# Optimization experiments

Measured on AMD Instinct MI355X. Metric: run time of the kernel, lower is better.

## Reference

```python
import jax, jax.numpy as jnp
import numpy as np

D = 32  # latent_dim
# relation order for stacked params: 0=ss, 1=tt, 2=st, 3=ts

def setup_inputs() -> dict:
    key = jax.random.key(0)
    ks = jax.random.split(key, 6)
    B, N, T = 32, 1024, 256
    spatial_nodes = jax.random.normal(ks[0], (B, N, D), dtype=jnp.float32)
    temporal_nodes = jax.random.normal(ks[1], (B, T, D), dtype=jnp.float32)
    # Linear(2D, 1) weights for the 4 relation MLPs and 4 mask MLPs, stacked.
    scale = 1.0 / np.sqrt(2 * D)
    W_rel = jax.random.uniform(ks[2], (4, 2 * D), jnp.float32, -scale, scale)
    b_rel = jax.random.uniform(ks[3], (4,), jnp.float32, -scale, scale)
    W_mask = jax.random.uniform(ks[4], (4, 2 * D), jnp.float32, -scale, scale)
    b_mask = jax.random.uniform(ks[5], (4,), jnp.float32, -scale, scale)
    return {"spatial_nodes": spatial_nodes, "temporal_nodes": temporal_nodes,
            "W_rel": W_rel, "b_rel": b_rel, "W_mask": W_mask, "b_mask": b_mask}


def _sub_graph(x1, x2, w_rel, brel, w_mask, bmask):
    # Linear applied to concat(x1_i, x2_j) decomposes as x1_i@w[:D] + x2_j@w[D:] + b,
    # avoiding the O(B*N1*N2*2D) concat intermediate of the original code.
    a1 = x1 @ w_rel[:D]          # [B, N1]
    a2 = x2 @ w_rel[D:]          # [B, N2]
    adj = a1[:, :, None] + a2[:, None, :] + brel   # [B, N1, N2]
    m1 = x1 @ w_mask[:D]
    m2 = x2 @ w_mask[D:]
    mask = jax.nn.relu(m1[:, :, None] + m2[:, None, :] + bmask)
    return adj, mask


def reference(spatial_nodes, temporal_nodes, W_rel, b_rel, W_mask, b_mask):
    s, t = spatial_nodes, temporal_nodes
    ss_a, ss_m = _sub_graph(s, s, W_rel[0], b_rel[0], W_mask[0], b_mask[0])
    tt_a, tt_m = _sub_graph(t, t, W_rel[1], b_rel[1], W_mask[1], b_mask[1])
    st_a, st_m = _sub_graph(s, t, W_rel[2], b_rel[2], W_mask[2], b_mask[2])
    ts_a, ts_m = _sub_graph(t, s, W_rel[3], b_rel[3], W_mask[3], b_mask[3])
    adj = jnp.concatenate([
        jnp.concatenate([ss_a, st_a], axis=-1),
        jnp.concatenate([ts_a, tt_a], axis=-1)], axis=-2)   # [B, N+T, N+T]
    mask = jnp.concatenate([
        jnp.concatenate([ss_m, st_m], axis=-1),
        jnp.concatenate([ts_m, tt_m], axis=-1)], axis=-2)
    adj = jnp.tanh(adj * mask)
    # Per-batch sparse edge extraction (nonzero/gather) in the original has
    # data-dependent shapes; it is a pure re-indexing of adj's nonzeros and is
    # omitted from the jit-compatible dense reference output.
    return adj
```

## Files before the change

### kernel.cpp

```cpp
#include <hip/hip_runtime.h>
#include <hip/hip_bf16.h>
#include <cstddef>

#define D_  32
#define N_  1024
#define T_  256
#define NT_ 1280
#define B_  32
#define TI  128
#define TJ  256

__device__ __forceinline__ float fast_tanh(float x) {
    float e = __expf(2.0f * x);
    return 1.0f - 2.0f * __builtin_amdgcn_rcpf(e + 1.0f);
}

__global__ __launch_bounds__(256) void mlp_adj_kernel(
    const float* __restrict__ S,  const float* __restrict__ Tn,
    const float* __restrict__ Wr, const float* __restrict__ br,
    const float* __restrict__ Wm, const float* __restrict__ bm,
    float* __restrict__ out)
{
    __shared__ float rowA[TI], rowM[TI], colA[TJ], colM[TJ];

    const int jt = blockIdx.x % (NT_ / TJ);
    const int it = (blockIdx.x / (NT_ / TJ)) % (NT_ / TI);
    const int b  = blockIdx.x / ((NT_ / TJ) * (NT_ / TI));
    const int i0 = it * TI, j0 = jt * TJ;
    const int rr = (i0 >= N_);
    const int cc = (j0 >= N_);
    const int r  = rr ? (cc ? 1 : 3) : (cc ? 2 : 0);

    const float* wrR = Wr + r * 2 * D_;
    const float* wrC = wrR + D_;
    const float* wmR = Wm + r * 2 * D_;
    const float* wmC = wmR + D_;
    const float  brel  = br[r];
    const float  bmask = bm[r];
    const int    tid   = threadIdx.x;

    const float* Xrow = rr ? (Tn + ((size_t)b * T_ + (i0 - N_)) * D_)
                           : (S  + ((size_t)b * N_ +  i0       ) * D_);
    const float* Xcol = cc ? (Tn + ((size_t)b * T_ + (j0 - N_)) * D_)
                           : (S  + ((size_t)b * N_ +  j0       ) * D_);

    if (tid < TI) {
        const float4* x  = (const float4*)(Xrow + (size_t)tid * D_);
        const float4* wa = (const float4*)wrR;
        const float4* wq = (const float4*)wmR;
        float aA = brel, aM = bmask;
        #pragma unroll
        for (int k = 0; k < D_ / 4; ++k) {
            float4 xv = x[k], av = wa[k], mv = wq[k];
            aA = fmaf(xv.x, av.x, aA); aM = fmaf(xv.x, mv.x, aM);
            aA = fmaf(xv.y, av.y, aA); aM = fmaf(xv.y, mv.y, aM);
            aA = fmaf(xv.z, av.z, aA); aM = fmaf(xv.z, mv.z, aM);
            aA = fmaf(xv.w, av.w, aA); aM = fmaf(xv.w, mv.w, aM);
        }
        rowA[tid] = aA; rowM[tid] = aM;
    }
    {
        const float4* x  = (const float4*)(Xcol + (size_t)tid * D_);
        const float4* wa = (const float4*)wrC;
        const float4* wq = (const float4*)wmC;
        float aA = 0.f, aM = 0.f;
        #pragma unroll
        for (int k = 0; k < D_ / 4; ++k) {
            float4 xv = x[k], av = wa[k], mv = wq[k];
            aA = fmaf(xv.x, av.x, aA); aM = fmaf(xv.x, mv.x, aM);
            aA = fmaf(xv.y, av.y, aA); aM = fmaf(xv.y, mv.y, aM);
            aA = fmaf(xv.z, av.z, aA); aM = fmaf(xv.z, mv.z, aM);
            aA = fmaf(xv.w, av.w, aA); aM = fmaf(xv.w, mv.w, aM);
        }
        colA[tid] = aA; colM[tid] = aM;
    }
    __syncthreads();

    const int jq = (tid & 63) * 4;
    const int rb = tid >> 6;
    const float4 cA = *(const float4*)&colA[jq];
    const float4 cM = *(const float4*)&colM[jq];
    float* outp = out + ((size_t)b * NT_ + i0) * NT_ + j0 + jq;

    for (int i = rb; i < TI; i += 4) {
        const float ra = rowA[i], rm = rowM[i];
        float4 o;
        o.x = fast_tanh((ra + cA.x) * fmaxf(rm + cM.x, 0.f));
        o.y = fast_tanh((ra + cA.y) * fmaxf(rm + cM.y, 0.f));
        o.z = fast_tanh((ra + cA.z) * fmaxf(rm + cM.z, 0.f));
        o.w = fast_tanh((ra + cA.w) * fmaxf(rm + cM.w, 0.f));
        *(float4*)(outp + (size_t)i * NT_) = o;
    }
}

extern "C" void kernel_launch(void* const* d_in, const int* in_sizes, int n_in,
                              void* d_out, int out_size, void* d_ws, size_t ws_size,
                              hipStream_t stream) {
    const float* S  = (const float*)d_in[0];
    const float* Tn = (const float*)d_in[1];
    const float* Wr = (const float*)d_in[2];
    const float* br = (const float*)d_in[3];
    const float* Wm = (const float*)d_in[4];
    const float* bm = (const float*)d_in[5];
    float* out = (float*)d_out;

    const int grid = B_ * (NT_ / TI) * (NT_ / TJ);
    mlp_adj_kernel<<<grid, 256, 0, stream>>>(S, Tn, Wr, br, Wm, bm, out);
}
```

Before: 218.2 us.

## Retile into full-width row bands with per-band column projections and nontemporal stores

```diff
diff --git a/kernel.cpp b/kernel.cpp
--- a/kernel.cpp
+++ b/kernel.cpp
@@ -1,5 +1,4 @@
 #include <hip/hip_runtime.h>
-#include <hip/hip_bf16.h>
 #include <cstddef>
 
 #define D_  32
@@ -7,12 +6,30 @@
 #define T_  256
 #define NT_ 1280
 #define B_  32
-#define TI  128
-#define TJ  256
+#define RB  32
+#define NBANDS (NT_/RB)
+
+typedef float vf4 __attribute__((ext_vector_type(4)));
 
 __device__ __forceinline__ float fast_tanh(float x) {
     float e = __expf(2.0f * x);
     return 1.0f - 2.0f * __builtin_amdgcn_rcpf(e + 1.0f);
+}
+
+__device__ __forceinline__ float dot32(const float* __restrict__ x,
+                                       const float* __restrict__ w) {
+    const float4* xv = (const float4*)x;
+    const float4* wv = (const float4*)w;
+    float a = 0.f;
+    #pragma unroll
+    for (int k = 0; k < D_ / 4; ++k) {
+        float4 xx = xv[k], ww = wv[k];
+        a = fmaf(xx.x, ww.x, a);
+        a = fmaf(xx.y, ww.y, a);
+        a = fmaf(xx.z, ww.z, a);
+        a = fmaf(xx.w, ww.w, a);
+    }
+    return a;
 }
 
 __global__ __launch_bounds__(256) void mlp_adj_kernel(
@@ -21,75 +38,82 @@
     const float* __restrict__ Wm, const float* __restrict__ bm,
     float* __restrict__ out)
 {
-    __shared__ float rowA[TI], rowM[TI], colA[TJ], colM[TJ];
+    __shared__ float colA[NT_], colM[NT_];
+    __shared__ float rowP[4][RB];
 
-    const int jt = blockIdx.x % (NT_ / TJ);
-    const int it = (blockIdx.x / (NT_ / TJ)) % (NT_ / TI);
-    const int b  = blockIdx.x / ((NT_ / TJ) * (NT_ / TI));
-    const int i0 = it * TI, j0 = jt * TJ;
-    const int rr = (i0 >= N_);
-    const int cc = (j0 >= N_);
-    const int r  = rr ? (cc ? 1 : 3) : (cc ? 2 : 0);
-
-    const float* wrR = Wr + r * 2 * D_;
-    const float* wrC = wrR + D_;
-    const float* wmR = Wm + r * 2 * D_;
-    const float* wmC = wmR + D_;
-    const float  brel  = br[r];
-    const float  bmask = bm[r];
-    const int    tid   = threadIdx.x;
+    const int band = blockIdx.x % NBANDS;
+    const int b    = blockIdx.x / NBANDS;
+    const int i0   = band * RB;
+    const int rr   = (i0 >= N_);
+    const int r1   = rr ? 3 : 0;
+    const int r2   = rr ? 1 : 2;
+    const int tid  = threadIdx.x;
 
     const float* Xrow = rr ? (Tn + ((size_t)b * T_ + (i0 - N_)) * D_)
-                           : (S  + ((size_t)b * N_ +  i0       ) * D_);
-    const float* Xcol = cc ? (Tn + ((size_t)b * T_ + (j0 - N_)) * D_)
-                           : (S  + ((size_t)b * N_ +  j0       ) * D_);
+                           : (S  + ((size_t)b * N_ +  i0      ) * D_);
 
-    if (tid < TI) {
-        const float4* x  = (const float4*)(Xrow + (size_t)tid * D_);
-        const float4* wa = (const float4*)wrR;
-        const float4* wq = (const float4*)wmR;
-        float aA = brel, aM = bmask;
+    if (tid < 4 * RB) {
+        const int i     = tid & (RB - 1);
+        const int which = tid >> 5;
+        const int rsel  = (which & 2) ? r2 : r1;
+        const float* w  = ((which & 1) ? Wm : Wr) + rsel * 2 * D_;
+        rowP[which][i] = dot32(Xrow + (size_t)i * D_, w);
+    }
+
+    {
+        const float* wrC1 = Wr + r1 * 2 * D_ + D_;
+        const float* wmC1 = Wm + r1 * 2 * D_ + D_;
+        const float* wrC2 = Wr + r2 * 2 * D_ + D_;
+        const float* wmC2 = Wm + r2 * 2 * D_ + D_;
+        const float  bA1 = br[r1], bM1 = bm[r1], bA2 = br[r2], bM2 = bm[r2];
         #pragma unroll
-        for (int k = 0; k < D_ / 4; ++k) {
-            float4 xv = x[k], av = wa[k], mv = wq[k];
-            aA = fmaf(xv.x, av.x, aA); aM = fmaf(xv.x, mv.x, aM);
-            aA = fmaf(xv.y, av.y, aA); aM = fmaf(xv.y, mv.y, aM);
-            aA = fmaf(xv.z, av.z, aA); aM = fmaf(xv.z, mv.z, aM);
-            aA = fmaf(xv.w, av.w, aA); aM = fmaf(xv.w, mv.w, aM);
+        for (int c = 0; c < 4; ++c) {
+            const int j = c * 256 + tid;
+            const float* xj = S + ((size_t)b * N_ + j) * D_;
+            colA[j] = dot32(xj, wrC1) + bA1;
+            colM[j] = dot32(xj, wmC1) + bM1;
         }
-        rowA[tid] = aA; rowM[tid] = aM;
-    }
-    {
-        const float4* x  = (const float4*)(Xcol + (size_t)tid * D_);
-        const float4* wa = (const float4*)wrC;
-        const float4* wq = (const float4*)wmC;
-        float aA = 0.f, aM = 0.f;
-        #pragma unroll
-        for (int k = 0; k < D_ / 4; ++k) {
-            float4 xv = x[k], av = wa[k], mv = wq[k];
-            aA = fmaf(xv.x, av.x, aA); aM = fmaf(xv.x, mv.x, aM);
-            aA = fmaf(xv.y, av.y, aA); aM = fmaf(xv.y, mv.y, aM);
-            aA = fmaf(xv.z, av.z, aA); aM = fmaf(xv.z, mv.z, aM);
-            aA = fmaf(xv.w, av.w, aA); aM = fmaf(xv.w, mv.w, aM);
+        {
+            const float* xj = Tn + ((size_t)b * T_ + tid) * D_;
+            colA[1024 + tid] = dot32(xj, wrC2) + bA2;
+            colM[1024 + tid] = dot32(xj, wmC2) + bM2;
         }
-        colA[tid] = aA; colM[tid] = aM;
     }
     __syncthreads();
 
-    const int jq = (tid & 63) * 4;
-    const int rb = tid >> 6;
-    const float4 cA = *(const float4*)&colA[jq];
-    const float4 cM = *(const float4*)&colM[jq];
-    float* outp = out + ((size_t)b * NT_ + i0) * NT_ + j0 + jq;
+    const int l = tid & 63;
+    const int w = tid >> 6;
+    float4 cAv[5], cMv[5];
+    #pragma unroll
+    for (int c = 0; c < 5; ++c) {
+        cAv[c] = *(const float4*)&colA[c * 256 + l * 4];
+        cMv[c] = *(const float4*)&colM[c * 256 + l * 4];
+    }
+    const int rbase = w * 8;
+    float rA1[8], rM1[8], rA2[8], rM2[8];
+    #pragma unroll
+    for (int k = 0; k < 8; ++k) {
+        rA1[k] = rowP[0][rbase + k];
+        rM1[k] = rowP[1][rbase + k];
+        rA2[k] = rowP[2][rbase + k];
+        rM2[k] = rowP[3][rbase + k];
+    }
 
-    for (int i = rb; i < TI; i += 4) {
-        const float ra = rowA[i], rm = rowM[i];
-        float4 o;
-        o.x = fast_tanh((ra + cA.x) * fmaxf(rm + cM.x, 0.f));
-        o.y = fast_tanh((ra + cA.y) * fmaxf(rm + cM.y, 0.f));
-        o.z = fast_tanh((ra + cA.z) * fmaxf(rm + cM.z, 0.f));
-        o.w = fast_tanh((ra + cA.w) * fmaxf(rm + cM.w, 0.f));
-        *(float4*)(outp + (size_t)i * NT_) = o;
+    float* outp = out + ((size_t)(b * NT_ + i0 + rbase)) * NT_ + l * 4;
+    #pragma unroll 2
+    for (int k = 0; k < 8; ++k) {
+        float* rp = outp + (size_t)k * NT_;
+        #pragma unroll
+        for (int c = 0; c < 5; ++c) {
+            const float ra = (c < 4) ? rA1[k] : rA2[k];
+            const float rm = (c < 4) ? rM1[k] : rM2[k];
+            vf4 o;
+            o.x = fast_tanh((ra + cAv[c].x) * fmaxf(rm + cMv[c].x, 0.f));
+            o.y = fast_tanh((ra + cAv[c].y) * fmaxf(rm + cMv[c].y, 0.f));
+            o.z = fast_tanh((ra + cAv[c].z) * fmaxf(rm + cMv[c].z, 0.f));
+            o.w = fast_tanh((ra + cAv[c].w) * fmaxf(rm + cMv[c].w, 0.f));
+            __builtin_nontemporal_store(o, (vf4*)(rp + c * 256));
+        }
     }
 }
 
@@ -104,6 +128,6 @@
     const float* bm = (const float*)d_in[5];
     float* out = (float*)d_out;
 
-    const int grid = B_ * (NT_ / TI) * (NT_ / TJ);
+    const int grid = B_ * NBANDS;
     mlp_adj_kernel<<<grid, 256, 0, stream>>>(S, Tn, Wr, br, Wm, bm, out);
 }
```

New measurement: 238.0 us. +9.1%, slower.

## Split into projection precompute kernel and row-per-block streaming epilogue kernel

Applied to the files above, without the earlier changes.

```diff
diff --git a/kernel.cpp b/kernel.cpp
--- a/kernel.cpp
+++ b/kernel.cpp
@@ -1,5 +1,4 @@
 #include <hip/hip_runtime.h>
-#include <hip/hip_bf16.h>
 #include <cstddef>
 
 #define D_  32
@@ -7,90 +6,96 @@
 #define T_  256
 #define NT_ 1280
 #define B_  32
-#define TI  128
-#define TJ  256
+
+#define RA_OFF 0
+#define RM_OFF (B_*NT_*2)
+#define CA_OFF (2*B_*NT_*2)
+#define CM_OFF (CA_OFF + 2*B_*NT_)
 
 __device__ __forceinline__ float fast_tanh(float x) {
     float e = __expf(2.0f * x);
     return 1.0f - 2.0f * __builtin_amdgcn_rcpf(e + 1.0f);
 }
 
-__global__ __launch_bounds__(256) void mlp_adj_kernel(
+__device__ __forceinline__ float dot8(const float4* __restrict__ xv,
+                                      const float* __restrict__ w) {
+    const float4* wv = (const float4*)w;
+    float a = 0.f;
+    #pragma unroll
+    for (int k = 0; k < D_ / 4; ++k) {
+        float4 ww = wv[k];
+        a = fmaf(xv[k].x, ww.x, a);
+        a = fmaf(xv[k].y, ww.y, a);
+        a = fmaf(xv[k].z, ww.z, a);
+        a = fmaf(xv[k].w, ww.w, a);
+    }
+    return a;
+}
+
+__global__ __launch_bounds__(256) void proj_kernel(
     const float* __restrict__ S,  const float* __restrict__ Tn,
     const float* __restrict__ Wr, const float* __restrict__ br,
     const float* __restrict__ Wm, const float* __restrict__ bm,
-    float* __restrict__ out)
+    float* __restrict__ ws)
 {
-    __shared__ float rowA[TI], rowM[TI], colA[TJ], colM[TJ];
+    const int idx = blockIdx.x * 256 + threadIdx.x;
+    const int b   = blockIdx.y;
+    const int seg = (idx >= N_);
+    const float* x = seg ? (Tn + ((size_t)b * T_ + (idx - N_)) * D_)
+                         : (S  + ((size_t)b * N_ +  idx      ) * D_);
+    float4 xv[D_ / 4];
+    #pragma unroll
+    for (int k = 0; k < D_ / 4; ++k) xv[k] = ((const float4*)x)[k];
 
-    const int jt = blockIdx.x % (NT_ / TJ);
-    const int it = (blockIdx.x / (NT_ / TJ)) % (NT_ / TI);
-    const int b  = blockIdx.x / ((NT_ / TJ) * (NT_ / TI));
-    const int i0 = it * TI, j0 = jt * TJ;
-    const int rr = (i0 >= N_);
-    const int cc = (j0 >= N_);
-    const int r  = rr ? (cc ? 1 : 3) : (cc ? 2 : 0);
+    const int rr0 = seg ? 3 : 0;
+    const int rr1 = seg ? 1 : 2;
+    float* RA = ws + RA_OFF;  float* RM = ws + RM_OFF;
+    const size_t ri = ((size_t)b * NT_ + idx) * 2;
+    RA[ri + 0] = dot8(xv, Wr + rr0 * 2 * D_) + br[rr0];
+    RA[ri + 1] = dot8(xv, Wr + rr1 * 2 * D_) + br[rr1];
+    RM[ri + 0] = dot8(xv, Wm + rr0 * 2 * D_) + bm[rr0];
+    RM[ri + 1] = dot8(xv, Wm + rr1 * 2 * D_) + bm[rr1];
 
-    const float* wrR = Wr + r * 2 * D_;
-    const float* wrC = wrR + D_;
-    const float* wmR = Wm + r * 2 * D_;
-    const float* wmC = wmR + D_;
-    const float  brel  = br[r];
-    const float  bmask = bm[r];
-    const int    tid   = threadIdx.x;
+    const int rc0 = seg ? 2 : 0;
+    const int rc1 = seg ? 1 : 3;
+    float* CA = ws + CA_OFF;  float* CM = ws + CM_OFF;
+    const size_t ci = (size_t)b * NT_ + idx;
+    CA[0 * B_ * NT_ + ci] = dot8(xv, Wr + rc0 * 2 * D_ + D_);
+    CA[1 * B_ * NT_ + ci] = dot8(xv, Wr + rc1 * 2 * D_ + D_);
+    CM[0 * B_ * NT_ + ci] = dot8(xv, Wm + rc0 * 2 * D_ + D_);
+    CM[1 * B_ * NT_ + ci] = dot8(xv, Wm + rc1 * 2 * D_ + D_);
+}
 
-    const float* Xrow = rr ? (Tn + ((size_t)b * T_ + (i0 - N_)) * D_)
-                           : (S  + ((size_t)b * N_ +  i0       ) * D_);
-    const float* Xcol = cc ? (Tn + ((size_t)b * T_ + (j0 - N_)) * D_)
-                           : (S  + ((size_t)b * N_ +  j0       ) * D_);
+__global__ __launch_bounds__(320) void epi_kernel(
+    const float* __restrict__ ws, float* __restrict__ out)
+{
+    const int tid   = threadIdx.x;
+    const int i     = blockIdx.x;
+    const int b     = blockIdx.y;
+    const int seg_i = (i   >= N_);
+    const int seg_j = (tid >= 256) ? 1 : 0;
 
-    if (tid < TI) {
-        const float4* x  = (const float4*)(Xrow + (size_t)tid * D_);
-        const float4* wa = (const float4*)wrR;
-        const float4* wq = (const float4*)wmR;
-        float aA = brel, aM = bmask;
-        #pragma unroll
-        for (int k = 0; k < D_ / 4; ++k) {
-            float4 xv = x[k], av = wa[k], mv = wq[k];
-            aA = fmaf(xv.x, av.x, aA); aM = fmaf(xv.x, mv.x, aM);
-            aA = fmaf(xv.y, av.y, aA); aM = fmaf(xv.y, mv.y, aM);
-            aA = fmaf(xv.z, av.z, aA); aM = fmaf(xv.z, mv.z, aM);
-            aA = fmaf(xv.w, av.w, aA); aM = fmaf(xv.w, mv.w, aM);
-        }
-        rowA[tid] = aA; rowM[tid] = aM;
-    }
-    {
-        const float4* x  = (const float4*)(Xcol + (size_t)tid * D_);
-        const float4* wa = (const float4*)wrC;
-        const float4* wq = (const float4*)wmC;
-        float aA = 0.f, aM = 0.f;
-        #pragma unroll
-        for (int k = 0; k < D_ / 4; ++k) {
-            float4 xv = x[k], av = wa[k], mv = wq[k];
-            aA = fmaf(xv.x, av.x, aA); aM = fmaf(xv.x, mv.x, aM);
-            aA = fmaf(xv.y, av.y, aA); aM = fmaf(xv.y, mv.y, aM);
-            aA = fmaf(xv.z, av.z, aA); aM = fmaf(xv.z, mv.z, aM);
-            aA = fmaf(xv.w, av.w, aA); aM = fmaf(xv.w, mv.w, aM);
-        }
-        colA[tid] = aA; colM[tid] = aM;
-    }
-    __syncthreads();
+    const float* RA = ws + RA_OFF;
+    const float* RM = ws + RM_OFF;
+    const float* CA = ws + CA_OFF;
+    const float* CM = ws + CM_OFF;
 
-    const int jq = (tid & 63) * 4;
-    const int rb = tid >> 6;
-    const float4 cA = *(const float4*)&colA[jq];
-    const float4 cM = *(const float4*)&colM[jq];
-    float* outp = out + ((size_t)b * NT_ + i0) * NT_ + j0 + jq;
+    const float2 rav = *(const float2*)&RA[((size_t)b * NT_ + i) * 2];
+    const float2 rmv = *(const float2*)&RM[((size_t)b * NT_ + i) * 2];
+    const float  ra  = seg_j ? rav.y : rav.x;
+    const float  rm  = seg_j ? rmv.y : rmv.x;
 
-    for (int i = rb; i < TI; i += 4) {
-        const float ra = rowA[i], rm = rowM[i];
-        float4 o;
-        o.x = fast_tanh((ra + cA.x) * fmaxf(rm + cM.x, 0.f));
-        o.y = fast_tanh((ra + cA.y) * fmaxf(rm + cM.y, 0.f));
-        o.z = fast_tanh((ra + cA.z) * fmaxf(rm + cM.z, 0.f));
-        o.w = fast_tanh((ra + cA.w) * fmaxf(rm + cM.w, 0.f));
-        *(float4*)(outp + (size_t)i * NT_) = o;
-    }
+    const int j = tid * 4;
+    const size_t cbase = ((size_t)seg_i * B_ + b) * NT_ + j;
+    const float4 ca = *(const float4*)&CA[cbase];
+    const float4 cm = *(const float4*)&CM[cbase];
+
+    float4 o;
+    o.x = fast_tanh((ra + ca.x) * fmaxf(rm + cm.x, 0.f));
+    o.y = fast_tanh((ra + ca.y) * fmaxf(rm + cm.y, 0.f));
+    o.z = fast_tanh((ra + ca.z) * fmaxf(rm + cm.z, 0.f));
+    o.w = fast_tanh((ra + ca.w) * fmaxf(rm + cm.w, 0.f));
+    *(float4*)(out + ((size_t)(b * NT_ + i)) * NT_ + j) = o;
 }
 
 extern "C" void kernel_launch(void* const* d_in, const int* in_sizes, int n_in,
@@ -103,7 +108,8 @@
     const float* Wm = (const float*)d_in[4];
     const float* bm = (const float*)d_in[5];
     float* out = (float*)d_out;
+    float* ws  = (float*)d_ws;
 
-    const int grid = B_ * (NT_ / TI) * (NT_ / TJ);
-    mlp_adj_kernel<<<grid, 256, 0, stream>>>(S, Tn, Wr, br, Wm, bm, out);
+    proj_kernel<<<dim3(NT_ / 256, B_), 256, 0, stream>>>(S, Tn, Wr, br, Wm, bm, ws);
+    epi_kernel <<<dim3(NT_, B_),       320, 0, stream>>>(ws, out);
 }
```

New measurement: 214.9 us. No clear change (-1.5%).
